# Kernel tuning notes

Hardware: AMD Instinct MI355X
Metric: run time of the kernel (lower is better)

## Reference

```python
import jax, jax.numpy as jnp
import numpy as np

N_U, N_V = 8192, 8192
IN_U, IN_V = 64, 64
OUT_U, OUT_V = 64, 64
RATING = 5


def setup_inputs() -> dict:
    key = jax.random.key(0)
    k1, k2, k3, k4, k5 = jax.random.split(key, 5)
    adj = jax.random.randint(k1, (N_U, N_V), 0, 6, dtype=jnp.int32)  # ratings 0..5, 0 = no edge
    u_feature = jax.random.normal(k2, (N_U, IN_U), dtype=jnp.float32)
    v_feature = jax.random.normal(k3, (N_V, IN_V), dtype=jnp.float32)
    weight_u = 0.02 * jax.random.normal(k4, (RATING, IN_V, OUT_U), dtype=jnp.float32)
    weight_v = 0.02 * jax.random.normal(k5, (RATING, IN_U, OUT_V), dtype=jnp.float32)
    return {"adj": adj, "u_feature": u_feature, "v_feature": v_feature,
            "weight_u": weight_u, "weight_v": weight_v}


def reference(adj, u_feature, v_feature, weight_u, weight_v):
    rating = weight_u.shape[0]
    dt = u_feature.dtype
    # Per-rating binary masks M_r: [R, n_u, n_v]
    ratings = jnp.arange(1, rating + 1, dtype=adj.dtype)
    masks = (adj[None, :, :] == ratings[:, None, None]).astype(dt)
    # Degree normalization (reciprocal of nonzero counts; inf -> 0)
    deg_u = jnp.sum(adj > 0, axis=1).astype(dt)  # [n_u]
    deg_v = jnp.sum(adj > 0, axis=0).astype(dt)  # [n_v]
    d_u = jnp.where(deg_u > 0, 1.0 / deg_u, 0.0)
    d_v = jnp.where(deg_v > 0, 1.0 / deg_v, 0.0)
    # Aggregate neighbor features per rating, project, sum over ratings.
    agg_u = jnp.einsum('ruv,vf->ruf', masks, v_feature)      # [R, n_u, in_v]
    out_u = jnp.einsum('ruf,rfo->uo', agg_u, weight_u)        # [n_u, out_u]
    out_u = d_u[:, None] * out_u
    agg_v = jnp.einsum('ruv,uf->rvf', masks, u_feature)      # [R, n_v, in_u]
    out_v = jnp.einsum('rvf,rfo->vo', agg_v, weight_v)        # [n_v, out_v]
    out_v = d_v[:, None] * out_v
    return (jax.nn.relu(out_u), jax.nn.relu(out_v))
```

## Files before the change

kernel.cpp:

```cpp
#include <hip/hip_runtime.h>

#define N_U 8192
#define N_V 8192
#define DIM 64
#define NR 5
#define BM 256
#define BK 512
#define NSTEP 16

typedef __attribute__((ext_vector_type(8))) short short8;
typedef __attribute__((ext_vector_type(4))) float f32x4;

__device__ inline unsigned short f2bf(float x) {
    unsigned u = __float_as_uint(x);
    return (unsigned short)((u + 0x7FFFu + ((u >> 16) & 1u)) >> 16);
}

__device__ inline size_t pfrag_idx(int r, int k, int o) {
    int ktile = k >> 5;
    int g     = (k >> 3) & 3;
    int j     = k & 7;
    int lane  = g * 16 + (o & 15);
    int n     = o >> 4;
    return ((((size_t)r * (N_V / 32) + ktile) * 4 + n) * 64 + lane) * 8 + j;
}

__global__ __launch_bounds__(256) void zero_k(float* __restrict__ outp,
                                              unsigned* __restrict__ deg)
{
    const int stride = gridDim.x * blockDim.x;
    int i = blockIdx.x * blockDim.x + threadIdx.x;
    int4 z = {0, 0, 0, 0};
    for (int idx = i; idx < 2 * N_U * DIM / 4; idx += stride) ((int4*)outp)[idx] = z;
    for (int idx = i; idx < (N_U + N_V) / 4; idx += stride) ((int4*)deg)[idx] = z;
}

__global__ __launch_bounds__(256) void precompute_P(
    const float* __restrict__ u_feat, const float* __restrict__ v_feat,
    const float* __restrict__ w_u, const float* __restrict__ w_v,
    unsigned short* __restrict__ p_u, unsigned short* __restrict__ p_v)
{
    int wid  = (blockIdx.x * blockDim.x + threadIdx.x) >> 6;
    int lane = threadIdx.x & 63;
    const int tasks = 2 * NR * (N_V / 32);
    if (wid >= tasks) return;
    int dir  = wid / (NR * (N_V / 32));
    int rem  = wid % (NR * (N_V / 32));
    int r    = rem / (N_V / 32);
    int v0   = (rem % (N_V / 32)) * 32;

    const float* feat = dir ? u_feat : v_feat;
    const float* w    = dir ? w_v : w_u;
    unsigned short* dst = dir ? p_v : p_u;

    float wreg[DIM];
#pragma unroll
    for (int f = 0; f < DIM; ++f) wreg[f] = w[(r * DIM + f) * DIM + lane];

    for (int v = v0; v < v0 + 32; ++v) {
        float x = feat[(size_t)v * DIM + lane];
        float acc = 0.f;
#pragma unroll
        for (int f = 0; f < DIM; ++f) acc += __shfl(x, f) * wreg[f];
        dst[pfrag_idx(r, v, lane)] = f2bf(acc);
    }
}

template <int TRANS>
__global__ __launch_bounds__(512, 4) void gemm_masked(
    const int* __restrict__ adj, const unsigned short* __restrict__ pfrag,
    float* __restrict__ outp, unsigned int* __restrict__ deg)
{
    __shared__ unsigned char tile[BM][256];
    __shared__ unsigned int  cnt[BM];

    const int tid  = threadIdx.x;
    const int lane = tid & 63;
    const int wv   = tid >> 6;
    const int b0   = blockIdx.x * BM;
    const int k0   = blockIdx.y * BK;

    unsigned cpack = 0;

    if (TRANS == 0) {
        int4 pre[4], nxt[4];
        const int sub = tid & 31;
        auto issue = [&](int rnd, int4* dst) {
            int row = rnd * 16 + (tid >> 5);
            const int* base = adj + (size_t)(b0 + row) * N_V + k0 + sub * 4;
#pragma unroll
            for (int it = 0; it < 4; ++it) dst[it] = *(const int4*)(base + it * 128);
        };
        issue(0, pre);
        for (int rnd = 0; rnd < 16; ++rnd) {
            if (rnd + 1 < 16) issue(rnd + 1, nxt);
            int row = rnd * 16 + (tid >> 5);
            unsigned lo = 0, hi = 0;
#pragma unroll
            for (int it = 0; it < 4; ++it) {
                int4 a = pre[it];
                unsigned long long bx = __ballot(a.x != 0), by = __ballot(a.y != 0);
                unsigned long long bz = __ballot(a.z != 0), bw = __ballot(a.w != 0);
                lo += __popcll(bx & 0xFFFFFFFFull) + __popcll(by & 0xFFFFFFFFull) +
                      __popcll(bz & 0xFFFFFFFFull) + __popcll(bw & 0xFFFFFFFFull);
                hi += __popcll(bx >> 32) + __popcll(by >> 32) +
                      __popcll(bz >> 32) + __popcll(bw >> 32);
                unsigned pk = (unsigned)a.x | ((unsigned)a.y << 4) |
                              ((unsigned)a.z << 8) | ((unsigned)a.w << 12);
                int d  = it * 16 + (sub >> 1);
                int dp = d ^ (row & 31);
                *(unsigned short*)&tile[row][dp * 4 + (sub & 1) * 2] = (unsigned short)pk;
            }
            if ((tid & 31) == 0) cnt[row] = (lane & 32) ? hi : lo;
#pragma unroll
            for (int it = 0; it < 4; ++it) pre[it] = nxt[it];
        }
    } else {
        const int v4 = (tid & 63) * 4;
        int4 pre[4], nxt[4];
        auto issue = [&](int rnd, int4* dst) {
            int u0 = rnd * 32 + (tid >> 6) * 4;
#pragma unroll
            for (int c = 0; c < 4; ++c)
                dst[c] = *(const int4*)(adj + (size_t)(k0 + u0 + c) * N_V + b0 + v4);
        };
        issue(0, pre);
        for (int rnd = 0; rnd < 16; ++rnd) {
            if (rnd + 1 < 16) issue(rnd + 1, nxt);
            const int* q0 = (const int*)&pre[0]; const int* q1 = (const int*)&pre[1];
            const int* q2 = (const int*)&pre[2]; const int* q3 = (const int*)&pre[3];
            int d    = rnd * 4 + ((tid >> 6) >> 1);
            int half = (tid >> 6) & 1;
#pragma unroll
            for (int cc = 0; cc < 4; ++cc) {
                int x0 = q0[cc], x1 = q1[cc], x2 = q2[cc], x3 = q3[cc];
                unsigned pk = (unsigned)x0 | ((unsigned)x1 << 4) |
                              ((unsigned)x2 << 8) | ((unsigned)x3 << 12);
                int row = v4 + cc;
                int dp  = d ^ (row & 31);
                *(unsigned short*)&tile[row][dp * 4 + half * 2] = (unsigned short)pk;
                cpack += (unsigned)((x0 != 0) + (x1 != 0) + (x2 != 0) + (x3 != 0)) << (8 * cc);
            }
#pragma unroll
            for (int c = 0; c < 4; ++c) pre[c] = nxt[c];
        }
    }
    __syncthreads();

    f32x4 acc[2][4];
#pragma unroll
    for (int m = 0; m < 2; ++m)
#pragma unroll
        for (int n = 0; n < 4; ++n) acc[m][n] = (f32x4){0.f, 0.f, 0.f, 0.f};

    const int mrow = wv * 32;
    for (int s = 0; s < NSTEP; ++s) {
        unsigned nib[2];
#pragma unroll
        for (int m = 0; m < 2; ++m) {
            int row = mrow + m * 16 + (lane & 15);
            int d   = s * 4 + (lane >> 4);
            nib[m] = *(const unsigned*)&tile[row][((d ^ (row & 31)) << 2)];
        }
        const int ktg = (k0 >> 5) + s;
#pragma unroll
        for (int r = 0; r < NR; ++r) {
            short8 bf[4];
#pragma unroll
            for (int n = 0; n < 4; ++n)
                bf[n] = *(const short8*)(pfrag +
                         ((((size_t)r * (N_V / 32) + ktg) * 4 + n) * 64 + lane) * 8);
            short8 am[2];
#pragma unroll
            for (int m = 0; m < 2; ++m)
#pragma unroll
                for (int j = 0; j < 8; ++j) {
                    unsigned nb = (nib[m] >> (4 * j)) & 0xFu;
                    am[m][j] = (short)(nb == (unsigned)(r + 1) ? 0x3F80 : 0);
                }
#pragma unroll
            for (int n = 0; n < 4; ++n) {
                acc[0][n] = __builtin_amdgcn_mfma_f32_16x16x32_bf16(am[0], bf[n], acc[0][n], 0, 0, 0);
                acc[1][n] = __builtin_amdgcn_mfma_f32_16x16x32_bf16(am[1], bf[n], acc[1][n], 0, 0, 0);
            }
        }
    }

#pragma unroll
    for (int m = 0; m < 2; ++m) {
        int rbase = b0 + mrow + m * 16 + ((lane >> 4) << 2);
#pragma unroll
        for (int n = 0; n < 4; ++n)
#pragma unroll
            for (int q = 0; q < 4; ++q)
                atomicAdd(&outp[(size_t)(rbase + q) * DIM + n * 16 + (lane & 15)], acc[m][n][q]);
    }

    if (TRANS == 0) {
        if (tid < BM) atomicAdd(&deg[b0 + tid], cnt[tid]);
    } else {
        __syncthreads();
        unsigned* sc = (unsigned*)&tile[0][0];
        sc[tid] = cpack;
        __syncthreads();
        if (tid < BM) {
            unsigned tot = 0;
            int base = tid >> 2, byte = tid & 3;
#pragma unroll
            for (int j = 0; j < 8; ++j) tot += (sc[j * 64 + base] >> (8 * byte)) & 0xFFu;
            atomicAdd(&deg[b0 + tid], tot);
        }
    }
}

__global__ __launch_bounds__(256) void finalize_k(
    float* __restrict__ outp, const unsigned int* __restrict__ deg_u,
    const unsigned int* __restrict__ deg_v)
{
    int idx = blockIdx.x * blockDim.x + threadIdx.x;
    const int total = 2 * N_U * DIM;
    for (; idx < total; idx += gridDim.x * blockDim.x) {
        int row = idx >> 6;
        unsigned d = (row < N_U) ? deg_u[row] : deg_v[row - N_U];
        float s = d ? (1.f / (float)d) : 0.f;
        float v = outp[idx] * s;
        outp[idx] = v > 0.f ? v : 0.f;
    }
}

extern "C" void kernel_launch(void* const* d_in, const int* in_sizes, int n_in,
                              void* d_out, int out_size, void* d_ws, size_t ws_size,
                              hipStream_t stream)
{
    const int*   adj = (const int*)d_in[0];
    const float* uf  = (const float*)d_in[1];
    const float* vf  = (const float*)d_in[2];
    const float* wu  = (const float*)d_in[3];
    const float* wv  = (const float*)d_in[4];
    float* outp = (float*)d_out;

    unsigned char* ws = (unsigned char*)d_ws;
    const size_t P_BYTES = (size_t)NR * (N_V / 32) * 4 * 64 * 8 * 2;
    unsigned short* p_u = (unsigned short*)ws;
    unsigned short* p_v = (unsigned short*)(ws + P_BYTES);
    unsigned int*   deg = (unsigned int*)(ws + 2 * P_BYTES);

    zero_k<<<1024, 256, 0, stream>>>(outp, deg);
    precompute_P<<<640, 256, 0, stream>>>(uf, vf, wu, wv, p_u, p_v);

    dim3 grid(N_U / BM, N_V / BK);
    gemm_masked<0><<<grid, 512, 0, stream>>>(adj, p_u, outp, deg);
    gemm_masked<1><<<grid, 512, 0, stream>>>(adj, p_v, outp + (size_t)N_U * DIM, deg + N_U);

    finalize_k<<<2048, 256, 0, stream>>>(outp, deg, deg + N_U);
}
```

Before: 282.7 us.

## Stage B fragments in LDS via async double-buffered loads; halve K tile

Each block now copies the per-rating projected feature fragments for every K step into a double-buffered LDS area using async global-to-LDS loads. The next step is prefetched while the current step runs its MFMAs, so every wave no longer fetches the same B fragments from global memory on its own. The K tile shrinks from 512 to 256, which gives twice as many blocks and twice the output atomics, and the degree count moves from ballots to shuffle reductions. It adds a barrier per step and more LDS use per block, which may limit occupancy.

```diff
diff --git a/kernel.cpp b/kernel.cpp
--- a/kernel.cpp
+++ b/kernel.cpp
@@ -1,12 +1,11 @@
 #include <hip/hip_runtime.h>
 
-#define N_U 8192
-#define N_V 8192
+#define NN 8192
 #define DIM 64
 #define NR 5
 #define BM 256
-#define BK 512
-#define NSTEP 16
+#define BK 256
+#define NSTEP 8
 
 typedef __attribute__((ext_vector_type(8))) short short8;
 typedef __attribute__((ext_vector_type(4))) float f32x4;
@@ -14,6 +13,12 @@
 __device__ inline unsigned short f2bf(float x) {
     unsigned u = __float_as_uint(x);
     return (unsigned short)((u + 0x7FFFu + ((u >> 16) & 1u)) >> 16);
+}
+
+__device__ __forceinline__ void gload_lds16(const void* g, void* l) {
+    __builtin_amdgcn_global_load_lds(
+        (const __attribute__((address_space(1))) void*)g,
+        (__attribute__((address_space(3))) void*)l, 16, 0, 0);
 }
 
 __device__ inline size_t pfrag_idx(int r, int k, int o) {
@@ -22,7 +27,7 @@
     int j     = k & 7;
     int lane  = g * 16 + (o & 15);
     int n     = o >> 4;
-    return ((((size_t)r * (N_V / 32) + ktile) * 4 + n) * 64 + lane) * 8 + j;
+    return ((((size_t)r * (NN / 32) + ktile) * 4 + n) * 64 + lane) * 8 + j;
 }
 
 __global__ __launch_bounds__(256) void zero_k(float* __restrict__ outp,
@@ -31,8 +36,8 @@
     const int stride = gridDim.x * blockDim.x;
     int i = blockIdx.x * blockDim.x + threadIdx.x;
     int4 z = {0, 0, 0, 0};
-    for (int idx = i; idx < 2 * N_U * DIM / 4; idx += stride) ((int4*)outp)[idx] = z;
-    for (int idx = i; idx < (N_U + N_V) / 4; idx += stride) ((int4*)deg)[idx] = z;
+    for (int idx = i; idx < 2 * NN * DIM / 4; idx += stride) ((int4*)outp)[idx] = z;
+    for (int idx = i; idx < 2 * NN / 4; idx += stride) ((int4*)deg)[idx] = z;
 }
 
 __global__ __launch_bounds__(256) void precompute_P(
@@ -42,12 +47,12 @@
 {
     int wid  = (blockIdx.x * blockDim.x + threadIdx.x) >> 6;
     int lane = threadIdx.x & 63;
-    const int tasks = 2 * NR * (N_V / 32);
+    const int tasks = 2 * NR * (NN / 32);
     if (wid >= tasks) return;
-    int dir  = wid / (NR * (N_V / 32));
-    int rem  = wid % (NR * (N_V / 32));
-    int r    = rem / (N_V / 32);
-    int v0   = (rem % (N_V / 32)) * 32;
+    int dir  = wid / (NR * (NN / 32));
+    int rem  = wid % (NR * (NN / 32));
+    int r    = rem / (NN / 32);
+    int v0   = (rem % (NN / 32)) * 32;
 
     const float* feat = dir ? u_feat : v_feat;
     const float* w    = dir ? w_v : w_u;
@@ -71,47 +76,60 @@
     const int* __restrict__ adj, const unsigned short* __restrict__ pfrag,
     float* __restrict__ outp, unsigned int* __restrict__ deg)
 {
-    __shared__ unsigned char tile[BM][256];
-    __shared__ unsigned int  cnt[BM];
+    __shared__ unsigned char  tile[BM][BK / 2];
+    __shared__ unsigned short bufB[2][NR * 4 * 512];
+    __shared__ unsigned int   cnt[BM];
 
     const int tid  = threadIdx.x;
     const int lane = tid & 63;
     const int wv   = tid >> 6;
     const int b0   = blockIdx.x * BM;
     const int k0   = blockIdx.y * BK;
+    const int kt0  = k0 >> 5;
 
     unsigned cpack = 0;
 
+    auto issueB = [&](int s) {
+        const int p = s & 1;
+        const int ktg = kt0 + s;
+        for (int c = wv; c < 20; c += 8) {
+            int r = c >> 2, n = c & 3;
+            const unsigned short* src =
+                pfrag + (((size_t)(r * (NN / 32) + ktg) * 4 + n) << 9) + lane * 8;
+            gload_lds16(src, (void*)&bufB[p][c << 9]);
+        }
+    };
+
+    issueB(0);
+
     if (TRANS == 0) {
+        const int sub = tid & 15;
+        const int rq  = tid >> 4;
         int4 pre[4], nxt[4];
-        const int sub = tid & 31;
         auto issue = [&](int rnd, int4* dst) {
-            int row = rnd * 16 + (tid >> 5);
-            const int* base = adj + (size_t)(b0 + row) * N_V + k0 + sub * 4;
-#pragma unroll
-            for (int it = 0; it < 4; ++it) dst[it] = *(const int4*)(base + it * 128);
+            int row = rnd * 32 + rq;
+            const int* base = adj + (size_t)(b0 + row) * NN + k0 + sub * 4;
+#pragma unroll
+            for (int it = 0; it < 4; ++it) dst[it] = *(const int4*)(base + it * 64);
         };
         issue(0, pre);
-        for (int rnd = 0; rnd < 16; ++rnd) {
-            if (rnd + 1 < 16) issue(rnd + 1, nxt);
-            int row = rnd * 16 + (tid >> 5);
-            unsigned lo = 0, hi = 0;
+        for (int rnd = 0; rnd < 8; ++rnd) {
+            if (rnd + 1 < 8) issue(rnd + 1, nxt);
+            int row = rnd * 32 + rq;
+            int c = 0;
 #pragma unroll
             for (int it = 0; it < 4; ++it) {
                 int4 a = pre[it];
-                unsigned long long bx = __ballot(a.x != 0), by = __ballot(a.y != 0);
-                unsigned long long bz = __ballot(a.z != 0), bw = __ballot(a.w != 0);
-                lo += __popcll(bx & 0xFFFFFFFFull) + __popcll(by & 0xFFFFFFFFull) +
-                      __popcll(bz & 0xFFFFFFFFull) + __popcll(bw & 0xFFFFFFFFull);
-                hi += __popcll(bx >> 32) + __popcll(by >> 32) +
-                      __popcll(bz >> 32) + __popcll(bw >> 32);
+                c += (a.x != 0) + (a.y != 0) + (a.z != 0) + (a.w != 0);
                 unsigned pk = (unsigned)a.x | ((unsigned)a.y << 4) |
                               ((unsigned)a.z << 8) | ((unsigned)a.w << 12);
-                int d  = it * 16 + (sub >> 1);
+                int d  = it * 8 + (sub >> 1);
                 int dp = d ^ (row & 31);
                 *(unsigned short*)&tile[row][dp * 4 + (sub & 1) * 2] = (unsigned short)pk;
             }
-            if ((tid & 31) == 0) cnt[row] = (lane & 32) ? hi : lo;
+            c += __shfl_xor(c, 1); c += __shfl_xor(c, 2);
+            c += __shfl_xor(c, 4); c += __shfl_xor(c, 8);
+            if (sub == 0) cnt[row] = (unsigned)c;
 #pragma unroll
             for (int it = 0; it < 4; ++it) pre[it] = nxt[it];
         }
@@ -119,18 +137,17 @@
         const int v4 = (tid & 63) * 4;
         int4 pre[4], nxt[4];
         auto issue = [&](int rnd, int4* dst) {
-            int u0 = rnd * 32 + (tid >> 6) * 4;
+            int u0 = rnd * 32 + wv * 4;
 #pragma unroll
             for (int c = 0; c < 4; ++c)
-                dst[c] = *(const int4*)(adj + (size_t)(k0 + u0 + c) * N_V + b0 + v4);
+                dst[c] = *(const int4*)(adj + (size_t)(k0 + u0 + c) * NN + b0 + v4);
         };
         issue(0, pre);
-        for (int rnd = 0; rnd < 16; ++rnd) {
-            if (rnd + 1 < 16) issue(rnd + 1, nxt);
+        for (int rnd = 0; rnd < 8; ++rnd) {
+            if (rnd + 1 < 8) issue(rnd + 1, nxt);
             const int* q0 = (const int*)&pre[0]; const int* q1 = (const int*)&pre[1];
             const int* q2 = (const int*)&pre[2]; const int* q3 = (const int*)&pre[3];
-            int d    = rnd * 4 + ((tid >> 6) >> 1);
-            int half = (tid >> 6) & 1;
+            int d = rnd * 4 + (wv >> 1);
 #pragma unroll
             for (int cc = 0; cc < 4; ++cc) {
                 int x0 = q0[cc], x1 = q1[cc], x2 = q2[cc], x3 = q3[cc];
@@ -138,7 +155,7 @@
                               ((unsigned)x2 << 8) | ((unsigned)x3 << 12);
                 int row = v4 + cc;
                 int dp  = d ^ (row & 31);
-                *(unsigned short*)&tile[row][dp * 4 + half * 2] = (unsigned short)pk;
+                *(unsigned short*)&tile[row][dp * 4 + (wv & 1) * 2] = (unsigned short)pk;
                 cpack += (unsigned)((x0 != 0) + (x1 != 0) + (x2 != 0) + (x3 != 0)) << (8 * cc);
             }
 #pragma unroll
@@ -153,37 +170,35 @@
 #pragma unroll
         for (int n = 0; n < 4; ++n) acc[m][n] = (f32x4){0.f, 0.f, 0.f, 0.f};
 
+    const unsigned* t32 = (const unsigned*)&tile[0][0];
     const int mrow = wv * 32;
+
     for (int s = 0; s < NSTEP; ++s) {
+        if (s + 1 < NSTEP) issueB(s + 1);
+        const int p = s & 1;
         unsigned nib[2];
 #pragma unroll
         for (int m = 0; m < 2; ++m) {
             int row = mrow + m * 16 + (lane & 15);
             int d   = s * 4 + (lane >> 4);
-            nib[m] = *(const unsigned*)&tile[row][((d ^ (row & 31)) << 2)];
-        }
-        const int ktg = (k0 >> 5) + s;
+            nib[m] = t32[row * 32 + (d ^ (row & 31))];
+        }
 #pragma unroll
         for (int r = 0; r < NR; ++r) {
-            short8 bf[4];
-#pragma unroll
-            for (int n = 0; n < 4; ++n)
-                bf[n] = *(const short8*)(pfrag +
-                         ((((size_t)r * (N_V / 32) + ktg) * 4 + n) * 64 + lane) * 8);
             short8 am[2];
 #pragma unroll
             for (int m = 0; m < 2; ++m)
 #pragma unroll
-                for (int j = 0; j < 8; ++j) {
-                    unsigned nb = (nib[m] >> (4 * j)) & 0xFu;
-                    am[m][j] = (short)(nb == (unsigned)(r + 1) ? 0x3F80 : 0);
-                }
+                for (int j = 0; j < 8; ++j)
+                    am[m][j] = (short)((((nib[m] >> (4 * j)) & 0xFu) == (unsigned)(r + 1)) ? 0x3F80 : 0);
 #pragma unroll
             for (int n = 0; n < 4; ++n) {
-                acc[0][n] = __builtin_amdgcn_mfma_f32_16x16x32_bf16(am[0], bf[n], acc[0][n], 0, 0, 0);
-                acc[1][n] = __builtin_amdgcn_mfma_f32_16x16x32_bf16(am[1], bf[n], acc[1][n], 0, 0, 0);
+                short8 bf = *(const short8*)&bufB[p][((r * 4 + n) << 9) + lane * 8];
+                acc[0][n] = __builtin_amdgcn_mfma_f32_16x16x32_bf16(am[0], bf, acc[0][n], 0, 0, 0);
+                acc[1][n] = __builtin_amdgcn_mfma_f32_16x16x32_bf16(am[1], bf, acc[1][n], 0, 0, 0);
             }
         }
+        __syncthreads();
     }
 
 #pragma unroll
@@ -199,7 +214,6 @@
     if (TRANS == 0) {
         if (tid < BM) atomicAdd(&deg[b0 + tid], cnt[tid]);
     } else {
-        __syncthreads();
         unsigned* sc = (unsigned*)&tile[0][0];
         sc[tid] = cpack;
         __syncthreads();
@@ -218,10 +232,10 @@
     const unsigned int* __restrict__ deg_v)
 {
     int idx = blockIdx.x * blockDim.x + threadIdx.x;
-    const int total = 2 * N_U * DIM;
+    const int total = 2 * NN * DIM;
     for (; idx < total; idx += gridDim.x * blockDim.x) {
         int row = idx >> 6;
-        unsigned d = (row < N_U) ? deg_u[row] : deg_v[row - N_U];
+        unsigned d = (row < NN) ? deg_u[row] : deg_v[row - NN];
         float s = d ? (1.f / (float)d) : 0.f;
         float v = outp[idx] * s;
         outp[idx] = v > 0.f ? v : 0.f;
@@ -240,7 +254,7 @@
     float* outp = (float*)d_out;
 
     unsigned char* ws = (unsigned char*)d_ws;
-    const size_t P_BYTES = (size_t)NR * (N_V / 32) * 4 * 64 * 8 * 2;
+    const size_t P_BYTES = (size_t)NR * (NN / 32) * 4 * 64 * 8 * 2;
     unsigned short* p_u = (unsigned short*)ws;
     unsigned short* p_v = (unsigned short*)(ws + P_BYTES);
     unsigned int*   deg = (unsigned int*)(ws + 2 * P_BYTES);
@@ -248,9 +262,9 @@
     zero_k<<<1024, 256, 0, stream>>>(outp, deg);
     precompute_P<<<640, 256, 0, stream>>>(uf, vf, wu, wv, p_u, p_v);
 
-    dim3 grid(N_U / BM, N_V / BK);
+    dim3 grid(NN / BM, NN / BK);
     gemm_masked<0><<<grid, 512, 0, stream>>>(adj, p_u, outp, deg);
-    gemm_masked<1><<<grid, 512, 0, stream>>>(adj, p_v, outp + (size_t)N_U * DIM, deg + N_U);
-
-    finalize_k<<<2048, 256, 0, stream>>>(outp, deg, deg + N_U);
-}
+    gemm_masked<1><<<grid, 512, 0, stream>>>(adj, p_v, outp + (size_t)NN * DIM, deg + NN);
+
+    finalize_k<<<2048, 256, 0, stream>>>(outp, deg, deg + NN);
+}
```

Measured after the change: 320.8 us. +13.5%, slower.

## Replace split-K float atomics with partial buffers and a vectorized reduction

Applied to the files above, without the earlier changes.

Each GEMM block now writes its split-K partial result to a dedicated workspace slice with plain stores instead of atomically adding into the output. A new reduce kernel sums the 16 partial slices per row, applies degree normalization and ReLU, and writes the output with float4 stores. This drops the output zeroing pass and the atomic contention on global memory. In exchange it adds about 64 MB of partial-buffer traffic (written once, read once) and a larger workspace requirement.

```diff
diff --git a/kernel.cpp b/kernel.cpp
--- a/kernel.cpp
+++ b/kernel.cpp
@@ -1,12 +1,12 @@
 #include <hip/hip_runtime.h>
 
-#define N_U 8192
-#define N_V 8192
+#define NN 8192
 #define DIM 64
 #define NR 5
 #define BM 256
 #define BK 512
 #define NSTEP 16
+#define NKC (NN / BK)
 
 typedef __attribute__((ext_vector_type(8))) short short8;
 typedef __attribute__((ext_vector_type(4))) float f32x4;
@@ -22,17 +22,13 @@
     int j     = k & 7;
     int lane  = g * 16 + (o & 15);
     int n     = o >> 4;
-    return ((((size_t)r * (N_V / 32) + ktile) * 4 + n) * 64 + lane) * 8 + j;
-}
-
-__global__ __launch_bounds__(256) void zero_k(float* __restrict__ outp,
-                                              unsigned* __restrict__ deg)
-{
-    const int stride = gridDim.x * blockDim.x;
+    return ((((size_t)r * (NN / 32) + ktile) * 4 + n) * 64 + lane) * 8 + j;
+}
+
+__global__ __launch_bounds__(256) void zero_k(unsigned* __restrict__ deg)
+{
     int i = blockIdx.x * blockDim.x + threadIdx.x;
-    int4 z = {0, 0, 0, 0};
-    for (int idx = i; idx < 2 * N_U * DIM / 4; idx += stride) ((int4*)outp)[idx] = z;
-    for (int idx = i; idx < (N_U + N_V) / 4; idx += stride) ((int4*)deg)[idx] = z;
+    if (i < 2 * NN) deg[i] = 0;
 }
 
 __global__ __launch_bounds__(256) void precompute_P(
@@ -42,12 +38,12 @@
 {
     int wid  = (blockIdx.x * blockDim.x + threadIdx.x) >> 6;
     int lane = threadIdx.x & 63;
-    const int tasks = 2 * NR * (N_V / 32);
+    const int tasks = 2 * NR * (NN / 32);
     if (wid >= tasks) return;
-    int dir  = wid / (NR * (N_V / 32));
-    int rem  = wid % (NR * (N_V / 32));
-    int r    = rem / (N_V / 32);
-    int v0   = (rem % (N_V / 32)) * 32;
+    int dir  = wid / (NR * (NN / 32));
+    int rem  = wid % (NR * (NN / 32));
+    int r    = rem / (NN / 32);
+    int v0   = (rem % (NN / 32)) * 32;
 
     const float* feat = dir ? u_feat : v_feat;
     const float* w    = dir ? w_v : w_u;
@@ -69,7 +65,7 @@
 template <int TRANS>
 __global__ __launch_bounds__(512, 4) void gemm_masked(
     const int* __restrict__ adj, const unsigned short* __restrict__ pfrag,
-    float* __restrict__ outp, unsigned int* __restrict__ deg)
+    float* __restrict__ part, unsigned int* __restrict__ deg)
 {
     __shared__ unsigned char tile[BM][256];
     __shared__ unsigned int  cnt[BM];
@@ -87,7 +83,7 @@
         const int sub = tid & 31;
         auto issue = [&](int rnd, int4* dst) {
             int row = rnd * 16 + (tid >> 5);
-            const int* base = adj + (size_t)(b0 + row) * N_V + k0 + sub * 4;
+            const int* base = adj + (size_t)(b0 + row) * NN + k0 + sub * 4;
 #pragma unroll
             for (int it = 0; it < 4; ++it) dst[it] = *(const int4*)(base + it * 128);
         };
@@ -122,7 +118,7 @@
             int u0 = rnd * 32 + (tid >> 6) * 4;
 #pragma unroll
             for (int c = 0; c < 4; ++c)
-                dst[c] = *(const int4*)(adj + (size_t)(k0 + u0 + c) * N_V + b0 + v4);
+                dst[c] = *(const int4*)(adj + (size_t)(k0 + u0 + c) * NN + b0 + v4);
         };
         issue(0, pre);
         for (int rnd = 0; rnd < 16; ++rnd) {
@@ -153,6 +149,7 @@
 #pragma unroll
         for (int n = 0; n < 4; ++n) acc[m][n] = (f32x4){0.f, 0.f, 0.f, 0.f};
 
+    const unsigned* t32 = (const unsigned*)&tile[0][0];
     const int mrow = wv * 32;
     for (int s = 0; s < NSTEP; ++s) {
         unsigned nib[2];
@@ -160,7 +157,7 @@
         for (int m = 0; m < 2; ++m) {
             int row = mrow + m * 16 + (lane & 15);
             int d   = s * 4 + (lane >> 4);
-            nib[m] = *(const unsigned*)&tile[row][((d ^ (row & 31)) << 2)];
+            nib[m] = t32[row * 64 + (d ^ (row & 31))];
         }
         const int ktg = (k0 >> 5) + s;
 #pragma unroll
@@ -169,7 +166,7 @@
 #pragma unroll
             for (int n = 0; n < 4; ++n)
                 bf[n] = *(const short8*)(pfrag +
-                         ((((size_t)r * (N_V / 32) + ktg) * 4 + n) * 64 + lane) * 8);
+                         ((((size_t)r * (NN / 32) + ktg) * 4 + n) * 64 + lane) * 8);
             short8 am[2];
 #pragma unroll
             for (int m = 0; m < 2; ++m)
@@ -186,6 +183,7 @@
         }
     }
 
+    float* pchunk = part + (size_t)blockIdx.y * NN * DIM;
 #pragma unroll
     for (int m = 0; m < 2; ++m) {
         int rbase = b0 + mrow + m * 16 + ((lane >> 4) << 2);
@@ -193,7 +191,7 @@
         for (int n = 0; n < 4; ++n)
 #pragma unroll
             for (int q = 0; q < 4; ++q)
-                atomicAdd(&outp[(size_t)(rbase + q) * DIM + n * 16 + (lane & 15)], acc[m][n][q]);
+                pchunk[(size_t)(rbase + q) * DIM + n * 16 + (lane & 15)] = acc[m][n][q];
     }
 
     if (TRANS == 0) {
@@ -213,18 +211,34 @@
     }
 }
 
-__global__ __launch_bounds__(256) void finalize_k(
-    float* __restrict__ outp, const unsigned int* __restrict__ deg_u,
-    const unsigned int* __restrict__ deg_v)
-{
-    int idx = blockIdx.x * blockDim.x + threadIdx.x;
-    const int total = 2 * N_U * DIM;
-    for (; idx < total; idx += gridDim.x * blockDim.x) {
+__global__ __launch_bounds__(256) void reduce_k(
+    const float* __restrict__ part_u, const float* __restrict__ part_v,
+    const unsigned int* __restrict__ deg,
+    float* __restrict__ outp)
+{
+    const int stride = gridDim.x * blockDim.x;
+    const int total4 = 2 * NN * DIM / 4;
+    for (int i4 = blockIdx.x * blockDim.x + threadIdx.x; i4 < total4; i4 += stride) {
+        int idx  = i4 * 4;
+        int half = idx >= NN * DIM;
+        const float* part = half ? part_v : part_u;
+        int off = idx - half * NN * DIM;
+        f32x4 sum = (f32x4){0.f, 0.f, 0.f, 0.f};
+#pragma unroll
+        for (int kc = 0; kc < NKC; ++kc) {
+            f32x4 p = *(const f32x4*)(part + (size_t)kc * NN * DIM + off);
+            sum += p;
+        }
         int row = idx >> 6;
-        unsigned d = (row < N_U) ? deg_u[row] : deg_v[row - N_U];
+        unsigned d = deg[row];
         float s = d ? (1.f / (float)d) : 0.f;
-        float v = outp[idx] * s;
-        outp[idx] = v > 0.f ? v : 0.f;
+        f32x4 o;
+#pragma unroll
+        for (int j = 0; j < 4; ++j) {
+            float v = sum[j] * s;
+            o[j] = v > 0.f ? v : 0.f;
+        }
+        *(f32x4*)(outp + idx) = o;
     }
 }
 
@@ -240,17 +254,20 @@
     float* outp = (float*)d_out;
 
     unsigned char* ws = (unsigned char*)d_ws;
-    const size_t P_BYTES = (size_t)NR * (N_V / 32) * 4 * 64 * 8 * 2;
-    unsigned short* p_u = (unsigned short*)ws;
-    unsigned short* p_v = (unsigned short*)(ws + P_BYTES);
-    unsigned int*   deg = (unsigned int*)(ws + 2 * P_BYTES);
-
-    zero_k<<<1024, 256, 0, stream>>>(outp, deg);
+    const size_t P_BYTES    = (size_t)NR * (NN / 32) * 4 * 64 * 8 * 2;
+    const size_t PART_BYTES = (size_t)NKC * NN * DIM * sizeof(float);
+    unsigned short* p_u    = (unsigned short*)ws;
+    unsigned short* p_v    = (unsigned short*)(ws + P_BYTES);
+    unsigned int*   deg    = (unsigned int*)(ws + 2 * P_BYTES);
+    float*          part_u = (float*)(ws + 2 * P_BYTES + 2 * NN * sizeof(unsigned));
+    float*          part_v = (float*)((unsigned char*)part_u + PART_BYTES);
+
+    zero_k<<<64, 256, 0, stream>>>(deg);
     precompute_P<<<640, 256, 0, stream>>>(uf, vf, wu, wv, p_u, p_v);
 
-    dim3 grid(N_U / BM, N_V / BK);
-    gemm_masked<0><<<grid, 512, 0, stream>>>(adj, p_u, outp, deg);
-    gemm_masked<1><<<grid, 512, 0, stream>>>(adj, p_v, outp + (size_t)N_U * DIM, deg + N_U);
-
-    finalize_k<<<2048, 256, 0, stream>>>(outp, deg, deg + N_U);
-}
+    dim3 grid(NN / BM, NKC);
+    gemm_masked<0><<<grid, 512, 0, stream>>>(adj, p_u, part_u, deg);
+    gemm_masked<1><<<grid, 512, 0, stream>>>(adj, p_v, part_v, deg + NN);
+
+    reduce_k<<<2048, 256, 0, stream>>>(part_u, part_v, deg, outp);
+}
```

Measured after the change: 294.2 us. 1.04x slower.
